# Optimization experiments

Measured on AMD Instinct MI355X. Metric: run time of the kernel, lower is better.

The kernel has to match this reference:

```python
import jax, jax.numpy as jnp
import numpy as np

ENTRY = 1024      # entry_size
TUPLE = 16        # tuple_size
NCLS = 10         # n_classes
BATCH = 4096
NNEU = ENTRY // TUPLE          # 64 neurons per discriminator
NADDR = 2 ** TUPLE             # 65536 RAM addresses per neuron
RAM_DENSITY = 0.3              # fraction of addresses seen during 'fit'


def setup_inputs() -> dict:
    key = jax.random.key(0)
    k1, k2, k3 = jax.random.split(key, 3)
    # binary input bits
    samples = jax.random.randint(k1, (BATCH, ENTRY), 0, 2, dtype=jnp.int32)
    # one random permutation of the entry bits per class (as in __init__)
    tuple_mapping = jax.vmap(lambda k: jax.random.permutation(k, ENTRY))(
        jax.random.split(k2, NCLS)
    ).astype(jnp.int64)
    # dense RAM membership table: ram[c, n, a] == 1.0 iff address a was
    # written into neuron n of discriminator c during fit()
    ram = (jax.random.uniform(k3, (NCLS, NNEU, NADDR)) < RAM_DENSITY).astype(jnp.float32)
    return {"samples": samples, "tuple_mapping": tuple_mapping, "ram": ram}


def reference(samples, tuple_mapping, ram):
    # samples: [B, E] binary int32; tuple_mapping: [C, E]; ram: [C, N, A]
    B = samples.shape[0]
    C, N, A = ram.shape
    T = tuple_mapping.shape[1] // N  # tuple_size
    # per-class bit remapping: [B, C, E]
    mapped = jnp.take(samples, tuple_mapping, axis=1)
    mapped = mapped.reshape(B, C, N, T)
    # big-endian bit packing: (bits << flip(arange(T))).sum(-1)
    weights = (jnp.int32(1) << jnp.arange(T - 1, -1, -1, dtype=jnp.int32))
    addr = jnp.sum(mapped * weights, axis=-1)  # [B, C, N] in [0, 2^T)
    # flat gather into the RAM table: out[b,c,n] = ram[c, n, addr[b,c,n]]
    base = (jnp.arange(C, dtype=jnp.int64)[:, None] * N
            + jnp.arange(N, dtype=jnp.int64)[None, :]) * A  # [C, N]
    gidx = addr.astype(jnp.int64) + base[None, :, :]
    hits = jnp.take(ram.reshape(-1), gidx)  # [B, C, N]
    # per-discriminator response: count of neurons whose address was trained
    return hits.sum(axis=-1)  # [B, C]
```

## Files before the change

kernel.cpp:

```cpp
#include <hip/hip_runtime.h>

#define B_TOT   4096
#define E_SZ    1024
#define T_SZ    16
#define N_CLS   10
#define N_NEU   64
#define N_ADDR  65536
#define RWORDS  (N_ADDR / 32)
#define RAMBITS_WORDS (N_CLS * N_NEU * RWORDS)
#define SBITS_WORDS   (B_TOT * (E_SZ / 32))
#define RAM_BLOCKS    (RAMBITS_WORDS / 256)
#define SB_BLOCKS     (SBITS_WORDS / 256)

__global__ __launch_bounds__(256) void pack_all(const float* __restrict__ ram,
                                                const int* __restrict__ samples,
                                                unsigned* __restrict__ rambits,
                                                unsigned* __restrict__ sbits) {
    int blk = blockIdx.x;
    int tid = threadIdx.x;
    if (blk < RAM_BLOCKS) {
        int word = blk * 256 + tid;
        const float4* in4 = (const float4*)ram;
        unsigned w = 0;
#pragma unroll
        for (int j = 0; j < 8; ++j) {
            float4 v = in4[(size_t)word * 8 + j];
            w |= (v.x != 0.0f ? 1u : 0u) << (4 * j + 0);
            w |= (v.y != 0.0f ? 1u : 0u) << (4 * j + 1);
            w |= (v.z != 0.0f ? 1u : 0u) << (4 * j + 2);
            w |= (v.w != 0.0f ? 1u : 0u) << (4 * j + 3);
        }
        rambits[word] = w;
    } else {
        int word = (blk - RAM_BLOCKS) * 256 + tid;
        const int4* in4 = (const int4*)samples;
        unsigned w = 0;
#pragma unroll
        for (int j = 0; j < 8; ++j) {
            int4 v = in4[(size_t)word * 8 + j];
            w |= (v.x != 0 ? 1u : 0u) << (4 * j + 0);
            w |= (v.y != 0 ? 1u : 0u) << (4 * j + 1);
            w |= (v.z != 0 ? 1u : 0u) << (4 * j + 2);
            w |= (v.w != 0 ? 1u : 0u) << (4 * j + 3);
        }
        sbits[word] = w;
    }
}

__global__ __launch_bounds__(512) void wisard_main(const unsigned* __restrict__ sbits,
                                                   const int* __restrict__ tmap,
                                                   const unsigned* __restrict__ rambits,
                                                   float* __restrict__ out) {
    __shared__ unsigned smp[64 * 33];
    __shared__ int red[512];

    int bid  = blockIdx.x;
    int work = (bid & 7) * 80 + (bid >> 3);
    int c     = work >> 6;
    int btile = work & 63;
    int tid = threadIdx.x;

    for (int i = tid; i < 64 * 32; i += 512) {
        int bl = i >> 5, w = i & 31;
        smp[bl * 33 + w] = sbits[(btile * 64 + bl) * 32 + w];
    }
    __syncthreads();

    int lane = tid & 63;
    int base = __builtin_amdgcn_readfirstlane((tid >> 6) * 8);
    const int* tw = tmap + c * 1024 + base * 16;
    const unsigned* ramw = rambits + ((size_t)c << 17) + ((size_t)base << 11);
    unsigned row = (unsigned)(lane * 33);

    int acc = 0;
    for (int nn = 0; nn < 8; ++nn) {
        unsigned addr = 0;
#pragma unroll
        for (int t = 0; t < 16; ++t) {
            int e = tw[nn * 16 + t];
            unsigned s = smp[row + (unsigned)(e >> 5)];
            addr = (addr << 1) | ((s >> (e & 31)) & 1u);
        }
        unsigned wrd = ramw[(nn << 11) + (addr >> 5)];
        acc += (int)((wrd >> (addr & 31u)) & 1u);
    }

    red[tid] = acc;
    __syncthreads();
    if (tid < 64) {
        int s = 0;
#pragma unroll
        for (int k = 0; k < 8; ++k) s += red[tid + 64 * k];
        out[(btile * 64 + tid) * N_CLS + c] = (float)s;
    }
}

extern "C" void kernel_launch(void* const* d_in, const int* in_sizes, int n_in,
                              void* d_out, int out_size, void* d_ws, size_t ws_size,
                              hipStream_t stream) {
    const int*   samples = (const int*)d_in[0];
    const int*   tmap    = (const int*)d_in[1];
    const float* ram     = (const float*)d_in[2];

    float* out = (float*)d_out;

    unsigned* rambits = (unsigned*)d_ws;
    unsigned* sbits   = rambits + RAMBITS_WORDS;

    pack_all<<<RAM_BLOCKS + SB_BLOCKS, 256, 0, stream>>>(ram, samples, rambits, sbits);
    wisard_main<<<640, 512, 0, stream>>>(sbits, tmap, rambits, out);
}
```

Baseline: 253.2 us.

## Gather directly from float RAM table instead of prepacking it into bits

Drops the pass that packed the whole 168 MB float RAM table into a bitmap every call, and instead gathers individual floats from the original table inside the main kernel. Address computation is split from the gathers so all eight loads per thread can be issued together, giving more memory-level parallelism. The trade is that the gathers are now scattered 4-byte reads into a large table with little cache reuse, in place of a streaming read of the full table.

Measured after the change: 257.8 us. About the same (+1.8%).

```diff
diff --git a/kernel.cpp b/kernel.cpp
--- a/kernel.cpp
+++ b/kernel.cpp
@@ -6,50 +6,28 @@
 #define N_CLS   10
 #define N_NEU   64
 #define N_ADDR  65536
-#define RWORDS  (N_ADDR / 32)
-#define RAMBITS_WORDS (N_CLS * N_NEU * RWORDS)
 #define SBITS_WORDS   (B_TOT * (E_SZ / 32))
-#define RAM_BLOCKS    (RAMBITS_WORDS / 256)
 #define SB_BLOCKS     (SBITS_WORDS / 256)
 
-__global__ __launch_bounds__(256) void pack_all(const float* __restrict__ ram,
-                                                const int* __restrict__ samples,
-                                                unsigned* __restrict__ rambits,
-                                                unsigned* __restrict__ sbits) {
-    int blk = blockIdx.x;
-    int tid = threadIdx.x;
-    if (blk < RAM_BLOCKS) {
-        int word = blk * 256 + tid;
-        const float4* in4 = (const float4*)ram;
-        unsigned w = 0;
+__global__ __launch_bounds__(256) void pack_samples(const int* __restrict__ samples,
+                                                    unsigned* __restrict__ sbits) {
+    int word = blockIdx.x * 256 + threadIdx.x;
+    const int4* in4 = (const int4*)samples;
+    unsigned w = 0;
 #pragma unroll
-        for (int j = 0; j < 8; ++j) {
-            float4 v = in4[(size_t)word * 8 + j];
-            w |= (v.x != 0.0f ? 1u : 0u) << (4 * j + 0);
-            w |= (v.y != 0.0f ? 1u : 0u) << (4 * j + 1);
-            w |= (v.z != 0.0f ? 1u : 0u) << (4 * j + 2);
-            w |= (v.w != 0.0f ? 1u : 0u) << (4 * j + 3);
-        }
-        rambits[word] = w;
-    } else {
-        int word = (blk - RAM_BLOCKS) * 256 + tid;
-        const int4* in4 = (const int4*)samples;
-        unsigned w = 0;
-#pragma unroll
-        for (int j = 0; j < 8; ++j) {
-            int4 v = in4[(size_t)word * 8 + j];
-            w |= (v.x != 0 ? 1u : 0u) << (4 * j + 0);
-            w |= (v.y != 0 ? 1u : 0u) << (4 * j + 1);
-            w |= (v.z != 0 ? 1u : 0u) << (4 * j + 2);
-            w |= (v.w != 0 ? 1u : 0u) << (4 * j + 3);
-        }
-        sbits[word] = w;
+    for (int j = 0; j < 8; ++j) {
+        int4 v = in4[(size_t)word * 8 + j];
+        w |= (v.x != 0 ? 1u : 0u) << (4 * j + 0);
+        w |= (v.y != 0 ? 1u : 0u) << (4 * j + 1);
+        w |= (v.z != 0 ? 1u : 0u) << (4 * j + 2);
+        w |= (v.w != 0 ? 1u : 0u) << (4 * j + 3);
     }
+    sbits[word] = w;
 }
 
 __global__ __launch_bounds__(512) void wisard_main(const unsigned* __restrict__ sbits,
                                                    const int* __restrict__ tmap,
-                                                   const unsigned* __restrict__ rambits,
+                                                   const float* __restrict__ ram,
                                                    float* __restrict__ out) {
     __shared__ unsigned smp[64 * 33];
     __shared__ int red[512];
@@ -69,20 +47,26 @@
     int lane = tid & 63;
     int base = __builtin_amdgcn_readfirstlane((tid >> 6) * 8);
     const int* tw = tmap + c * 1024 + base * 16;
-    const unsigned* ramw = rambits + ((size_t)c << 17) + ((size_t)base << 11);
+    const float* ramw = ram + ((size_t)c << 22) + ((size_t)base << 16);
     unsigned row = (unsigned)(lane * 33);
 
-    int acc = 0;
+    unsigned addr[8];
+#pragma unroll
     for (int nn = 0; nn < 8; ++nn) {
-        unsigned addr = 0;
+        unsigned a = 0;
 #pragma unroll
         for (int t = 0; t < 16; ++t) {
             int e = tw[nn * 16 + t];
             unsigned s = smp[row + (unsigned)(e >> 5)];
-            addr = (addr << 1) | ((s >> (e & 31)) & 1u);
+            a = (a << 1) | ((s >> (e & 31)) & 1u);
         }
-        unsigned wrd = ramw[(nn << 11) + (addr >> 5)];
-        acc += (int)((wrd >> (addr & 31u)) & 1u);
+        addr[nn] = a;
+    }
+    int acc = 0;
+#pragma unroll
+    for (int nn = 0; nn < 8; ++nn) {
+        float v = ramw[((size_t)nn << 16) + addr[nn]];
+        acc += (v != 0.0f) ? 1 : 0;
     }
 
     red[tid] = acc;
@@ -104,9 +88,8 @@
 
     float* out = (float*)d_out;
 
-    unsigned* rambits = (unsigned*)d_ws;
-    unsigned* sbits   = rambits + RAMBITS_WORDS;
+    unsigned* sbits = (unsigned*)d_ws;
 
-    pack_all<<<RAM_BLOCKS + SB_BLOCKS, 256, 0, stream>>>(ram, samples, rambits, sbits);
-    wisard_main<<<640, 512, 0, stream>>>(sbits, tmap, rambits, out);
+    pack_samples<<<SB_BLOCKS, 256, 0, stream>>>(samples, sbits);
+    wisard_main<<<640, 512, 0, stream>>>(sbits, tmap, ram, out);
 }
```
